# Kernel tuning notes

Measured on AMD Instinct MI355X. Metric: run time of the kernel, lower is better.

Reference implementation:

```python
import jax, jax.numpy as jnp
import numpy as np

N, F = 10000, 64
EDGE_PROB = 0.003  # sparse 0/1 adjacency, stored dense as in the original
LEAKY_SLOPE = 0.01
ELU_ALPHA = 1.0


def setup_inputs() -> dict:
    key = jax.random.key(0)
    ks = jax.random.split(key, 8)
    x = jax.random.normal(ks[0], (N, F), dtype=jnp.float32)
    # symmetric 0/1 adjacency (edge_index was concatenated with its flip)
    u = jax.random.uniform(ks[1], (N, N))
    A = (u < EDGE_PROB).astype(jnp.float32)
    A = jnp.maximum(A, A.T)
    dims = [F, 16, 32, 16, 32, 8]
    Ws = [jax.random.normal(ks[2 + i], (dims[i], dims[i + 1]), dtype=jnp.float32)
          * (1.0 / np.sqrt(dims[i])) for i in range(5)]
    return {"x": x, "A": A, "W0": Ws[0], "W1": Ws[1], "W2": Ws[2], "W3": Ws[3], "W4": Ws[4]}


def reference(x, A, W0, W1, W2, W3, W4):
    # layer s: temp = A @ h ; ahw = temp @ W[s] ; h = act(ahw)
    t1 = A @ x
    a1 = t1 @ W0
    h1 = jax.nn.relu(a1)

    t2 = A @ h1
    a2 = t2 @ W1
    h2 = jax.nn.silu(a2)  # swish

    t3 = A @ h2
    a3 = t3 @ W2
    h3 = jax.nn.elu(a3, alpha=ELU_ALPHA)

    t4 = A @ h3
    a4 = t4 @ W3
    h4 = jnp.where(a4 >= 0, a4, LEAKY_SLOPE * a4)  # leaky relu

    t5 = A @ h4
    a5 = t5 @ W4
    z = jax.nn.sigmoid(a5)

    # original returns (ah, ahw, z); flatten the lists into a tuple
    return (t1, t2, t3, t4, t5, a1, a2, a3, a4, a5, z)
```

## Files before the change

### kernel.cpp

```cpp
#include <hip/hip_runtime.h>
#include <math.h>

#define N_NODES 10000
#define NCH 40
#define NQ4 2500
#define CAPR 128
#define WCAP 64

typedef float f32x4 __attribute__((ext_vector_type(4)));

template <int ACT>
__device__ __forceinline__ float activate(float v) {
    if (ACT == 0) return fmaxf(v, 0.0f);
    if (ACT == 1) return v / (1.0f + __expf(-v));
    if (ACT == 2) return (v >= 0.0f) ? v : (__expf(v) - 1.0f);
    if (ACT == 3) return (v >= 0.0f) ? v : 0.01f * v;
    return 1.0f / (1.0f + __expf(-v));
}

__global__ void zero_cl(int* __restrict__ cl) {
    const int i = blockIdx.x * blockDim.x + threadIdx.x;
    if (i < N_NODES) cl[i] = 0;
}

__global__ __launch_bounds__(256) void scan_upper_inv(
        const float* __restrict__ A,
        int* __restrict__ cu, int* __restrict__ colsU,
        int* __restrict__ cl, int* __restrict__ colsL) {
    __shared__ int sidx[4][WCAP];
    __shared__ int scnt[4];

    const int w    = threadIdx.x >> 6;
    const int lane = threadIdx.x & 63;
    const int row  = blockIdx.x;
    const int c0   = row >> 8;
    const int lo   = row & 255;

    const f32x4* __restrict__ arow = (const f32x4*)(A + (size_t)row * N_NODES);

    int cnt = 0;
    int c = c0 + w;
    f32x4 vc = (f32x4)(0.0f);
    if (c < NCH) {
        const int idx = c * 64 + lane;
        if (idx < NQ4) vc = __builtin_nontemporal_load(&arow[idx]);
    }
    while (c < NCH) {
        const int cn = c + 4;
        f32x4 vn = (f32x4)(0.0f);
        if (cn < NCH) {
            const int idxn = cn * 64 + lane;
            if (idxn < NQ4) vn = __builtin_nontemporal_load(&arow[idxn]);
        }
        if (c == c0) {
#pragma unroll
            for (int cc = 0; cc < 4; ++cc)
                if (4 * lane + cc < lo) vc[cc] = 0.0f;
        }
#pragma unroll
        for (int cc = 0; cc < 4; ++cc) {
            unsigned long long m = __ballot(vc[cc] != 0.0f);
            while (m) {
                const int b = __ffsll(m) - 1;
                m &= m - 1ull;
                if (lane == 0 && cnt < WCAP)
                    sidx[w][cnt] = 256 * c + 4 * b + cc;
                ++cnt;
            }
        }
        vc = vn;
        c = cn;
    }
    if (cnt > WCAP) cnt = WCAP;
    if (lane == 0) scnt[w] = cnt;
    __syncthreads();

    const int s0 = scnt[0], s1 = scnt[1], s2 = scnt[2], s3 = scnt[3];
    const int offs[4] = {0, s0, s0 + s1, s0 + s1 + s2};
    int total = s0 + s1 + s2 + s3;
    if (total > CAPR) total = CAPR;

    const int mycnt = scnt[w];
    if (lane < mycnt) {
        const int p = offs[w] + lane;
        const int tgt = sidx[w][lane];
        if (p < CAPR) colsU[row * CAPR + p] = tgt;
        if (tgt != row) {
            const int pos = atomicAdd(&cl[tgt], 1);
            if (pos < CAPR) colsL[tgt * CAPR + pos] = row;
        }
    }
    if (threadIdx.x == 0) cu[row] = total;
}

__global__ __launch_bounds__(256) void sort_gather_l1(
        const float* __restrict__ x, const float* __restrict__ W0,
        int* __restrict__ cl, int* __restrict__ colsL,
        const int* __restrict__ cu, const int* __restrict__ colsU,
        float* __restrict__ t1, float* __restrict__ a1,
        float* __restrict__ h1) {
    __shared__ int   sl[4][128];
    __shared__ float st[4][64];

    const int w    = threadIdx.x >> 6;
    const int lane = threadIdx.x & 63;
    const int row  = blockIdx.x * 4 + w;

    int n = cl[row];
    if (n > CAPR) n = CAPR;
    sl[w][lane]      = (lane < n)      ? colsL[row * CAPR + lane]      : 0x7FFFFFFF;
    sl[w][lane + 64] = (lane + 64 < n) ? colsL[row * CAPR + lane + 64] : 0x7FFFFFFF;
    __syncthreads();

    for (int size = 2; size <= 128; size <<= 1) {
        for (int stride = size >> 1; stride > 0; stride >>= 1) {
            const int i = ((lane & ~(stride - 1)) << 1) | (lane & (stride - 1));
            const int j = i | stride;
            const int a = sl[w][i], b = sl[w][j];
            const bool asc = (i & size) == 0;
            const bool doswap = asc ? (a > b) : (a < b);
            if (doswap) { sl[w][i] = b; sl[w][j] = a; }
            __syncthreads();
        }
    }

    if (lane < n)      colsL[row * CAPR + lane]      = sl[w][lane];
    if (lane + 64 < n) colsL[row * CAPR + lane + 64] = sl[w][lane + 64];
    if (lane == 0) cl[row] = n;

    const int du = cu[row];
    const int dt = n + du;
    const f32x4* __restrict__ x4 = (const f32x4*)x;
    const int f4 = lane & 15;
    const int g  = lane >> 4;

    f32x4 acc = (f32x4)(0.0f);
    int k = g;
    for (; k + 12 < dt; k += 16) {
        const int j0 = (k      < n) ? sl[w][k]      : colsU[row * CAPR + k - n];
        const int j1 = (k + 4  < n) ? sl[w][k + 4]  : colsU[row * CAPR + k + 4 - n];
        const int j2 = (k + 8  < n) ? sl[w][k + 8]  : colsU[row * CAPR + k + 8 - n];
        const int j3 = (k + 12 < n) ? sl[w][k + 12] : colsU[row * CAPR + k + 12 - n];
        acc += x4[j0 * 16 + f4];
        acc += x4[j1 * 16 + f4];
        acc += x4[j2 * 16 + f4];
        acc += x4[j3 * 16 + f4];
    }
    for (; k < dt; k += 4) {
        const int j = (k < n) ? sl[w][k] : colsU[row * CAPR + k - n];
        acc += x4[j * 16 + f4];
    }
#pragma unroll
    for (int cc = 0; cc < 4; ++cc) {
        acc[cc] += __shfl_xor(acc[cc], 16);
        acc[cc] += __shfl_xor(acc[cc], 32);
    }
    if (g == 0) {
        *(f32x4*)&st[w][f4 * 4] = acc;
        *(f32x4*)&t1[row * 64 + f4 * 4] = acc;
    }

    const int o = lane & 15, q = lane >> 4;
    float a = 0.0f;
#pragma unroll
    for (int i = 0; i < 16; ++i) {
        const int ff = q * 16 + i;
        a += st[w][ff] * W0[ff * 16 + o];
    }
    a += __shfl_xor(a, 16);
    a += __shfl_xor(a, 32);
    if (q == 0) {
        a1[row * 16 + o] = a;
        h1[row * 16 + o] = activate<0>(a);
    }
}

template <int FIN, int FOUT, int ACT>
__global__ __launch_bounds__(256) void layer_fused(
        const int* __restrict__ cl, const int* __restrict__ colsL,
        const int* __restrict__ cu, const int* __restrict__ colsU,
        const float* __restrict__ h_in, const float* __restrict__ W,
        float* __restrict__ t_out, float* __restrict__ a_out,
        float* __restrict__ h_out) {
    constexpr int LPR = FIN / 4;
    constexpr int G   = 64 / LPR;
    __shared__ float tls[4][FIN];
    const int w    = threadIdx.x >> 6;
    const int lane = threadIdx.x & 63;
    const int row  = blockIdx.x * 4 + w;

    const int f4 = lane % LPR;
    const int g  = lane / LPR;
    int dl = cl[row]; if (dl > CAPR) dl = CAPR;
    const int du = cu[row];
    const int* __restrict__ crowL = colsL + row * CAPR;
    const int* __restrict__ crowU = colsU + row * CAPR;
    const f32x4* __restrict__ h4 = (const f32x4*)h_in;

    f32x4 acc = (f32x4)(0.0f);
#pragma unroll 4
    for (int k = g; k < dl; k += G)
        acc += h4[crowL[k] * LPR + f4];
#pragma unroll 4
    for (int k = g; k < du; k += G)
        acc += h4[crowU[k] * LPR + f4];
#pragma unroll
    for (int off = LPR; off < 64; off <<= 1) {
#pragma unroll
        for (int cc = 0; cc < 4; ++cc)
            acc[cc] += __shfl_xor(acc[cc], off);
    }
    if (g == 0) {
        *(f32x4*)&tls[w][f4 * 4] = acc;
        *(f32x4*)&t_out[row * FIN + f4 * 4] = acc;
    }
    __syncthreads();

    constexpr int NQP = 64 / FOUT;
    constexpr int K   = FIN / NQP;
    const int o = lane % FOUT, q = lane / FOUT;
    float a = 0.0f;
#pragma unroll
    for (int i = 0; i < K; ++i) {
        const int ff = q * K + i;
        a += tls[w][ff] * W[ff * FOUT + o];
    }
#pragma unroll
    for (int off = FOUT; off < 64; off <<= 1)
        a += __shfl_xor(a, off);
    if (q == 0) {
        a_out[row * FOUT + o] = a;
        h_out[row * FOUT + o] = activate<ACT>(a);
    }
}

extern "C" void kernel_launch(void* const* d_in, const int* in_sizes, int n_in,
                              void* d_out, int out_size, void* d_ws, size_t ws_size,
                              hipStream_t stream) {
    const float* x  = (const float*)d_in[0];
    const float* A  = (const float*)d_in[1];
    const float* W0 = (const float*)d_in[2];
    const float* W1 = (const float*)d_in[3];
    const float* W2 = (const float*)d_in[4];
    const float* W3 = (const float*)d_in[5];
    const float* W4 = (const float*)d_in[6];

    float* out = (float*)d_out;
    float* t1 = out + 0;
    float* t2 = out + 640000;
    float* t3 = out + 800000;
    float* t4 = out + 1120000;
    float* t5 = out + 1280000;
    float* a1 = out + 1600000;
    float* a2 = out + 1760000;
    float* a3 = out + 2080000;
    float* a4 = out + 2240000;
    float* a5 = out + 2560000;
    float* z  = out + 2640000;

    char* ws = (char*)d_ws;
    int*   cu    = (int*)ws;
    int*   cl    = (int*)(ws + (size_t)1 * 1024 * 1024);
    int*   colsU = (int*)(ws + (size_t)2 * 1024 * 1024);
    int*   colsL = (int*)(ws + (size_t)8 * 1024 * 1024);
    float* hA    = (float*)(ws + (size_t)14 * 1024 * 1024);
    float* hB    = (float*)(ws + (size_t)16 * 1024 * 1024);

    zero_cl<<<40, 256, 0, stream>>>(cl);

    scan_upper_inv<<<N_NODES, 256, 0, stream>>>(A, cu, colsU, cl, colsL);

    sort_gather_l1<<<2500, 256, 0, stream>>>(x, W0, cl, colsL, cu, colsU,
                                             t1, a1, hA);

    layer_fused<16, 32, 1><<<2500, 256, 0, stream>>>(cl, colsL, cu, colsU,
                                                     hA, W1, t2, a2, hB);
    layer_fused<32, 16, 2><<<2500, 256, 0, stream>>>(cl, colsL, cu, colsU,
                                                     hB, W2, t3, a3, hA);
    layer_fused<16, 32, 3><<<2500, 256, 0, stream>>>(cl, colsL, cu, colsU,
                                                     hA, W3, t4, a4, hB);
    layer_fused<32, 8, 4><<<2500, 256, 0, stream>>>(cl, colsL, cu, colsU,
                                                    hB, W4, t5, a5, z);
}
```

Baseline: 116.2 us.

## Replace atomic scatter and bitonic sort with upper-triangle bitmap transpose

```diff
diff --git a/kernel.cpp b/kernel.cpp
--- a/kernel.cpp
+++ b/kernel.cpp
@@ -6,8 +6,11 @@
 #define NQ4 2500
 #define CAPR 128
 #define WCAP 64
+#define BW 160
+#define RT 157
 
 typedef float f32x4 __attribute__((ext_vector_type(4)));
+typedef unsigned long long u64;
 
 template <int ACT>
 __device__ __forceinline__ float activate(float v) {
@@ -18,15 +21,10 @@
     return 1.0f / (1.0f + __expf(-v));
 }
 
-__global__ void zero_cl(int* __restrict__ cl) {
-    const int i = blockIdx.x * blockDim.x + threadIdx.x;
-    if (i < N_NODES) cl[i] = 0;
-}
-
-__global__ __launch_bounds__(256) void scan_upper_inv(
+__global__ __launch_bounds__(256) void scan_upper(
         const float* __restrict__ A,
         int* __restrict__ cu, int* __restrict__ colsU,
-        int* __restrict__ cl, int* __restrict__ colsL) {
+        u64* __restrict__ bm) {
     __shared__ int sidx[4][WCAP];
     __shared__ int scnt[4];
 
@@ -37,19 +35,23 @@
     const int lo   = row & 255;
 
     const f32x4* __restrict__ arow = (const f32x4*)(A + (size_t)row * N_NODES);
+    u64* __restrict__ bmrow = bm + (size_t)row * BW;
+
+    const int nch = NCH - c0;
+    const int b0  = c0 + (nch * w) / 4;
+    const int b1  = c0 + (nch * (w + 1)) / 4;
 
     int cnt = 0;
-    int c = c0 + w;
+    int c = b0;
     f32x4 vc = (f32x4)(0.0f);
-    if (c < NCH) {
+    if (c < b1) {
         const int idx = c * 64 + lane;
         if (idx < NQ4) vc = __builtin_nontemporal_load(&arow[idx]);
     }
-    while (c < NCH) {
-        const int cn = c + 4;
+    while (c < b1) {
         f32x4 vn = (f32x4)(0.0f);
-        if (cn < NCH) {
-            const int idxn = cn * 64 + lane;
+        if (c + 1 < b1) {
+            const int idxn = (c + 1) * 64 + lane;
             if (idxn < NQ4) vn = __builtin_nontemporal_load(&arow[idxn]);
         }
         if (c == c0) {
@@ -57,9 +59,12 @@
             for (int cc = 0; cc < 4; ++cc)
                 if (4 * lane + cc < lo) vc[cc] = 0.0f;
         }
+        u64 mk0, mk1, mk2, mk3;
 #pragma unroll
         for (int cc = 0; cc < 4; ++cc) {
-            unsigned long long m = __ballot(vc[cc] != 0.0f);
+            u64 m = __ballot(vc[cc] != 0.0f);
+            if (cc == 0) mk0 = m; else if (cc == 1) mk1 = m;
+            else if (cc == 2) mk2 = m; else mk3 = m;
             while (m) {
                 const int b = __ffsll(m) - 1;
                 m &= m - 1ull;
@@ -68,8 +73,11 @@
                 ++cnt;
             }
         }
+        const u64 mw = (lane == 0) ? mk0 : (lane == 1) ? mk1
+                     : (lane == 2) ? mk2 : mk3;
+        if (lane < 4) bmrow[c * 4 + lane] = mw;
         vc = vn;
-        c = cn;
+        ++c;
     }
     if (cnt > WCAP) cnt = WCAP;
     if (lane == 0) scnt[w] = cnt;
@@ -79,57 +87,94 @@
     const int offs[4] = {0, s0, s0 + s1, s0 + s1 + s2};
     int total = s0 + s1 + s2 + s3;
     if (total > CAPR) total = CAPR;
-
-    const int mycnt = scnt[w];
-    if (lane < mycnt) {
+    if (lane < scnt[w]) {
         const int p = offs[w] + lane;
-        const int tgt = sidx[w][lane];
-        if (p < CAPR) colsU[row * CAPR + p] = tgt;
-        if (tgt != row) {
-            const int pos = atomicAdd(&cl[tgt], 1);
-            if (pos < CAPR) colsL[tgt * CAPR + pos] = row;
-        }
+        if (p < CAPR) colsU[row * CAPR + p] = sidx[w][lane];
     }
     if (threadIdx.x == 0) cu[row] = total;
 }
 
-__global__ __launch_bounds__(256) void sort_gather_l1(
-        const float* __restrict__ x, const float* __restrict__ W0,
+__device__ __forceinline__ void emit_tile(u64 wl, int C, int R, int lane,
+                                          u64* __restrict__ tt) {
+    u64 myword = 0;
+#pragma unroll 8
+    for (int q = 0; q < 64; ++q) {
+        const u64 res = __ballot(((wl >> q) & 1ull) != 0ull);
+        if (lane == q) myword = res;
+    }
+    tt[((size_t)C * RT + R) * 64 + lane] = myword;
+}
+
+__global__ __launch_bounds__(256) void bit_transpose(
+        const u64* __restrict__ bm, u64* __restrict__ tt) {
+    const int R    = blockIdx.x;
+    const int w    = threadIdx.x >> 6;
+    const int lane = threadIdx.x & 63;
+    const u64* __restrict__ src = bm + ((size_t)R * 64 + lane) * BW + w * 40;
+
+    u64 b0 = src[0], b1 = src[1], b2 = src[2], b3 = src[3];
+    const int Cb = w * 40;
+    for (int i = 0; i < 40; i += 4) {
+        const u64 w0 = b0, w1 = b1, w2 = b2, w3 = b3;
+        if (i + 4 < 40) {
+            b0 = src[i + 4]; b1 = src[i + 5];
+            b2 = src[i + 6]; b3 = src[i + 7];
+        }
+        emit_tile(w0, Cb + i,     R, lane, tt);
+        emit_tile(w1, Cb + i + 1, R, lane, tt);
+        emit_tile(w2, Cb + i + 2, R, lane, tt);
+        emit_tile(w3, Cb + i + 3, R, lane, tt);
+    }
+}
+
+__global__ __launch_bounds__(256) void extract_gather_l1(
+        const u64* __restrict__ tt, const float* __restrict__ x,
+        const float* __restrict__ W0,
+        const int* __restrict__ cu, const int* __restrict__ colsU,
         int* __restrict__ cl, int* __restrict__ colsL,
-        const int* __restrict__ cu, const int* __restrict__ colsU,
         float* __restrict__ t1, float* __restrict__ a1,
         float* __restrict__ h1) {
-    __shared__ int   sl[4][128];
+    __shared__ int   slw[4][CAPR];
     __shared__ float st[4][64];
 
     const int w    = threadIdx.x >> 6;
     const int lane = threadIdx.x & 63;
     const int row  = blockIdx.x * 4 + w;
 
-    int n = cl[row];
-    if (n > CAPR) n = CAPR;
-    sl[w][lane]      = (lane < n)      ? colsL[row * CAPR + lane]      : 0x7FFFFFFF;
-    sl[w][lane + 64] = (lane + 64 < n) ? colsL[row * CAPR + lane + 64] : 0x7FFFFFFF;
-    __syncthreads();
-
-    for (int size = 2; size <= 128; size <<= 1) {
-        for (int stride = size >> 1; stride > 0; stride >>= 1) {
-            const int i = ((lane & ~(stride - 1)) << 1) | (lane & (stride - 1));
-            const int j = i | stride;
-            const int a = sl[w][i], b = sl[w][j];
-            const bool asc = (i & size) == 0;
-            const bool doswap = asc ? (a > b) : (a < b);
-            if (doswap) { sl[w][i] = b; sl[w][j] = a; }
-            __syncthreads();
-        }
-    }
-
-    if (lane < n)      colsL[row * CAPR + lane]      = sl[w][lane];
-    if (lane + 64 < n) colsL[row * CAPR + lane + 64] = sl[w][lane + 64];
-    if (lane == 0) cl[row] = n;
+    const int C  = ((row >> 8) << 2) | (row & 3);
+    const int qq = (row >> 2) & 63;
+    const int rB = row >> 6;
+
+    int cnt = 0;
+    for (int rb = 0; rb <= rB; rb += 64) {
+        const int r = rb + lane;
+        u64 wd = 0;
+        if (r <= rB) wd = tt[((size_t)C * RT + r) * 64 + qq];
+        if (r == rB) wd &= ((1ull << (row & 63)) - 1ull);
+        const int pc = __popcll(wd);
+        int v = pc;
+#pragma unroll
+        for (int off = 1; off < 64; off <<= 1) {
+            const int t = __shfl_up(v, off);
+            if (lane >= off) v += t;
+        }
+        int base = cnt + v - pc;
+        u64 m = wd;
+        while (m) {
+            const int b = __ffsll(m) - 1;
+            m &= m - 1ull;
+            if (base < CAPR) slw[w][base] = r * 64 + b;
+            ++base;
+        }
+        cnt += __shfl(v, 63);
+    }
+    if (cnt > CAPR) cnt = CAPR;
+
+    for (int k = lane; k < cnt; k += 64) colsL[row * CAPR + k] = slw[w][k];
+    if (lane == 0) cl[row] = cnt;
 
     const int du = cu[row];
-    const int dt = n + du;
+    const int dt = cnt + du;
     const f32x4* __restrict__ x4 = (const f32x4*)x;
     const int f4 = lane & 15;
     const int g  = lane >> 4;
@@ -137,17 +182,17 @@
     f32x4 acc = (f32x4)(0.0f);
     int k = g;
     for (; k + 12 < dt; k += 16) {
-        const int j0 = (k      < n) ? sl[w][k]      : colsU[row * CAPR + k - n];
-        const int j1 = (k + 4  < n) ? sl[w][k + 4]  : colsU[row * CAPR + k + 4 - n];
-        const int j2 = (k + 8  < n) ? sl[w][k + 8]  : colsU[row * CAPR + k + 8 - n];
-        const int j3 = (k + 12 < n) ? sl[w][k + 12] : colsU[row * CAPR + k + 12 - n];
+        const int j0 = (k      < cnt) ? slw[w][k]      : colsU[row * CAPR + k - cnt];
+        const int j1 = (k + 4  < cnt) ? slw[w][k + 4]  : colsU[row * CAPR + k + 4 - cnt];
+        const int j2 = (k + 8  < cnt) ? slw[w][k + 8]  : colsU[row * CAPR + k + 8 - cnt];
+        const int j3 = (k + 12 < cnt) ? slw[w][k + 12] : colsU[row * CAPR + k + 12 - cnt];
         acc += x4[j0 * 16 + f4];
         acc += x4[j1 * 16 + f4];
         acc += x4[j2 * 16 + f4];
         acc += x4[j3 * 16 + f4];
     }
     for (; k < dt; k += 4) {
-        const int j = (k < n) ? sl[w][k] : colsU[row * CAPR + k - n];
+        const int j = (k < cnt) ? slw[w][k] : colsU[row * CAPR + k - cnt];
         acc += x4[j * 16 + f4];
     }
 #pragma unroll
@@ -259,19 +304,21 @@
     float* z  = out + 2640000;
 
     char* ws = (char*)d_ws;
-    int*   cu    = (int*)ws;
-    int*   cl    = (int*)(ws + (size_t)1 * 1024 * 1024);
-    int*   colsU = (int*)(ws + (size_t)2 * 1024 * 1024);
-    int*   colsL = (int*)(ws + (size_t)8 * 1024 * 1024);
-    float* hA    = (float*)(ws + (size_t)14 * 1024 * 1024);
-    float* hB    = (float*)(ws + (size_t)16 * 1024 * 1024);
-
-    zero_cl<<<40, 256, 0, stream>>>(cl);
-
-    scan_upper_inv<<<N_NODES, 256, 0, stream>>>(A, cu, colsU, cl, colsL);
-
-    sort_gather_l1<<<2500, 256, 0, stream>>>(x, W0, cl, colsL, cu, colsU,
-                                             t1, a1, hA);
+    u64*   bm    = (u64*)ws;
+    u64*   tt    = (u64*)(ws + 12861440);
+    int*   cu    = (int*)(ws + 25722880);
+    int*   cl    = (int*)(ws + 25762880);
+    int*   colsU = (int*)(ws + 25802880);
+    int*   colsL = (int*)(ws + 30922880);
+    float* hA    = (float*)(ws + 36042880);
+    float* hB    = (float*)(ws + 37322880);
+
+    scan_upper<<<N_NODES, 256, 0, stream>>>(A, cu, colsU, bm);
+
+    bit_transpose<<<RT, 256, 0, stream>>>(bm, tt);
+
+    extract_gather_l1<<<2500, 256, 0, stream>>>(tt, x, W0, cu, colsU,
+                                                cl, colsL, t1, a1, hA);
 
     layer_fused<16, 32, 1><<<2500, 256, 0, stream>>>(cl, colsL, cu, colsU,
                                                      hA, W1, t2, a2, hB);
```

After: 177.0 us. 52.4% more time.
